# Performance work log

Hardware: AMD Instinct MI355X
Metric: run time of the kernel (lower is better)

The kernel has to match this reference:

```python
import jax, jax.numpy as jnp
import numpy as np

H = 1024; NH = 16; L = 4; K = 128; N = 65536
ADIM_MOVE = 9; ADIM_TURN = 4; S = 2 * K + 2


def setup_inputs() -> dict:
    key = jax.random.key(0)
    ks = jax.random.split(key, 24)
    s = 0.02
    d = {}
    d['x'] = jax.random.normal(ks[0], (1, H), jnp.float32)
    d['memory_vectors'] = jax.random.normal(ks[1], (N, H), jnp.float32)
    d['memory_next_vectors'] = jax.random.normal(ks[2], (N, H), jnp.float32)
    d['memory_surprises'] = jax.random.uniform(ks[3], (N,), jnp.float32)
    d['memory_rewards'] = jax.random.normal(ks[4], (N,), jnp.float32)
    d['rand_noise'] = jax.random.uniform(ks[5], (N,), jnp.float32)
    d['action_idx_move'] = jax.random.randint(ks[6], (N,), 0, ADIM_MOVE)
    d['action_idx_turn'] = jax.random.randint(ks[7], (N,), 0, ADIM_TURN)
    d['start_token'] = jax.random.uniform(ks[8], (1, H)) * 2 - 1
    d['pos_emb'] = jax.random.uniform(ks[9], (S, H)) * 2 - 1
    d['in_proj_w'] = jax.random.normal(ks[10], (L, 3 * H, H)) * s
    d['in_proj_b'] = jnp.zeros((L, 3 * H))
    d['out_w'] = jax.random.normal(ks[11], (L, H, H)) * s
    d['out_b'] = jnp.zeros((L, H))
    d['ln1_w'] = jnp.ones((L, H)); d['ln1_b'] = jnp.zeros((L, H))
    d['ln2_w'] = jnp.ones((L, H)); d['ln2_b'] = jnp.zeros((L, H))
    d['ffn_w1'] = jax.random.normal(ks[12], (L, 4 * H, H)) * s
    d['ffn_b1'] = jnp.zeros((L, 4 * H))
    d['ffn_w2'] = jax.random.normal(ks[13], (L, H, 4 * H)) * s
    d['ffn_b2'] = jnp.zeros((L, H))
    d['act_move_w1'] = jax.random.normal(ks[14], (H, ADIM_MOVE)) * s
    d['act_move_b1'] = jnp.zeros((H,))
    d['act_move_w2'] = jax.random.normal(ks[15], (H, H)) * s
    d['act_move_b2'] = jnp.zeros((H,))
    d['act_turn_w1'] = jax.random.normal(ks[16], (H, ADIM_TURN)) * s
    d['act_turn_b1'] = jnp.zeros((H,))
    d['act_turn_w2'] = jax.random.normal(ks[17], (H, H)) * s
    d['act_turn_b2'] = jnp.zeros((H,))
    d['vh_w1'] = jax.random.normal(ks[18], (4 * H, H)) * s
    d['vh_b1'] = jnp.zeros((4 * H,))
    d['vh_w2'] = jax.random.normal(ks[19], (1, 4 * H)) * s
    d['vh_b2'] = jnp.zeros((1,))
    return d


def _get_scores(v):
    # tie-aware average rank / N (matches torch unique_consecutive logic)
    srt = jnp.sort(v)
    left = jnp.searchsorted(srt, v, side='left')
    right = jnp.searchsorted(srt, v, side='right')
    return ((left + right - 1).astype(v.dtype) / 2) / v.shape[0]


def _ln(x, w, b):
    m = x.mean(-1, keepdims=True)
    var = ((x - m) ** 2).mean(-1, keepdims=True)
    return (x - m) / jnp.sqrt(var + 1e-5) * w + b


def _gelu(x):
    return jax.nn.gelu(x, approximate=False)


def _mha(x, wqkv, bqkv, wo, bo, mask):
    dh = H // NH
    qkv = x @ wqkv.T + bqkv                      # [S, 3H]
    q, k, v = jnp.split(qkv, 3, axis=-1)
    q = q.reshape(-1, NH, dh); k = k.reshape(-1, NH, dh); v = v.reshape(-1, NH, dh)
    att = jnp.einsum('qhd,khd->hqk', q, k) / np.sqrt(dh).astype(np.float32)
    att = jax.nn.softmax(att + mask, axis=-1)
    o = jnp.einsum('hqk,khd->qhd', att, v).reshape(-1, H)
    return o @ wo.T + bo


def reference(x, memory_vectors, memory_next_vectors, memory_surprises, memory_rewards, rand_noise, action_idx_move, action_idx_turn, start_token, pos_emb, in_proj_w, in_proj_b, out_w, out_b, ln1_w, ln1_b, ln2_w, ln2_b, ffn_w1, ffn_b1, ffn_w2, ffn_b2, act_move_w1, act_move_b1, act_move_w2, act_move_b2, act_turn_w1, act_turn_b1, act_turn_w2, act_turn_b2, vh_w1, vh_b1, vh_w2, vh_b2):
    eps = 1e-8
    # ---- scoring (no_grad in original) ----
    xs = jax.lax.stop_gradient(x)
    xn = xs / jnp.maximum(jnp.linalg.norm(xs, axis=-1, keepdims=True), eps)
    mn = memory_vectors / jnp.maximum(jnp.linalg.norm(memory_vectors, axis=-1, keepdims=True), eps)
    sim = mn @ xn[0]                              # [N]
    scores = _get_scores(memory_surprises) ** 2 + _get_scores(sim) ** 2 + _get_scores(rand_noise) ** 2
    _, idx = jax.lax.top_k(scores, K)             # [K]
    # ---- gather memories + action one-hots ----
    sel = jax.lax.stop_gradient(memory_vectors[idx])   # [K, H]
    oh_move = jax.nn.one_hot(action_idx_move[idx], ADIM_MOVE, dtype=x.dtype)
    oh_turn = jax.nn.one_hot(action_idx_turn[idx], ADIM_TURN, dtype=x.dtype)
    av_move = _gelu(oh_move @ act_move_w1.T + act_move_b1) @ act_move_w2.T + act_move_b2
    av_turn = _gelu(oh_turn @ act_turn_w1.T + act_turn_b1) @ act_turn_w2.T + act_turn_b2
    av = (av_move + av_turn) / 2                  # mean over actions
    # interleave [v0, a0, v1, a1, ...], prepend start, append target
    vecs = jnp.stack((sel, av), axis=1).reshape(-1, H)
    vecs = jnp.concatenate((start_token, vecs, x), axis=0)   # [S, H]
    vecs = vecs + pos_emb
    mask = jnp.where(jnp.tril(jnp.ones((S, S), bool)), 0.0, -jnp.inf).astype(x.dtype)
    for l in range(L):
        vecs = vecs + _mha(_ln(vecs, ln1_w[l], ln1_b[l]), in_proj_w[l], in_proj_b[l], out_w[l], out_b[l], mask)
        h = _ln(vecs, ln2_w[l], ln2_b[l])
        vecs = vecs + _gelu(h @ ffn_w1[l].T + ffn_b1[l]) @ ffn_w2[l].T + ffn_b2[l]
    vidx = jnp.arange(K + 1) * 2 + 1
    vh_in = vecs[vidx]
    vp = _gelu(vh_in @ vh_w1.T + vh_b1) @ vh_w2.T + vh_b2   # [K+1, 1]
    sel_rewards = memory_rewards[idx]
    losses = (vp[:-1].ravel() - sel_rewards) ** 2            # mse, reduction='none'
    return (vecs[1:], memory_next_vectors[idx], vp[-1], losses, sel_rewards)
```

## Files before the change

### kernel.cpp

```cpp
#include <hip/hip_runtime.h>
#include <hip/hip_bf16.h>
#include <math.h>
#include <stdint.h>

typedef unsigned int u32;
typedef unsigned short u16;
typedef unsigned long long u64;

#define NM   65536
#define HD   1024
#define KS   128
#define SQ   258
#define NL   4
#define NBIN 65536
#define CCAP 2048

using bf16x8 = __attribute__((ext_vector_type(8))) short;
using f32x4v = __attribute__((ext_vector_type(4))) float;

static constexpr size_t A256(size_t x){ return (x + 255) & ~(size_t)255; }

constexpr size_t OFF_H3   = 0;
constexpr size_t OFF_C3   = OFF_H3 + (size_t)3*NBIN*4;
constexpr size_t OFF_HS   = OFF_C3 + (size_t)3*NBIN*4;
constexpr size_t ZERO_BYTES = OFF_HS + (size_t)NBIN*4;
constexpr u32 ZBLK = 1792;
constexpr size_t OFF_BS   = A256(ZERO_BYTES);
constexpr size_t OFF_P3   = A256(OFF_BS + 192*4);
constexpr size_t OFF_K3   = A256(OFF_P3 + (size_t)3*(NBIN+1)*4);
constexpr size_t OFF_L3   = A256(OFF_K3 + (size_t)3*NM*4);
constexpr size_t OFF_KSC  = A256(OFF_L3 + (size_t)3*NM*2);
constexpr size_t OFF_IDX  = A256(OFF_KSC + (size_t)NM*4);
constexpr size_t OFF_REW  = A256(OFF_IDX  + (size_t)KS*4);
constexpr size_t OFF_HM   = A256(OFF_REW  + (size_t)KS*4);
constexpr size_t OFF_HT   = A256(OFF_HM   + (size_t)KS*HD*2);
constexpr size_t OFF_VECS = A256(OFF_HT   + (size_t)KS*HD*2);
// ... 209 lines not shown
      if(cum + c >= (u32)KS){ thrT = (u32)(base+j) << 16; cnt = 0; break; }
      cum += c;
    }
  }
  __syncthreads();
  u32 T = thrT;
  for(int i=t;i<NM;i+=1024){
    u32 k = keysS[i];
    if(k >= T){
      u32 p = atomicAdd(&cnt, 1u);
      if(p < (u32)CCAP) sm[p] = ((u64)(~k) << 32) | (u32)i;
    }
  }
  __syncthreads();
  u32 n = cnt; if(n > (u32)CCAP) n = CCAP;
  for(int i=t;i<CCAP;i+=1024) if(i >= (int)n) sm[i] = 0xFFFFFFFFFFFFFFFFull;
  __syncthreads();
  for(int k=2;k<=CCAP;k<<=1){
    for(int j=k>>1;j>0;j>>=1){
      for(int i=t;i<CCAP;i+=1024){
        int ixj = i ^ j;
        if(ixj > i){
          bool up = ((i & k) == 0);
          u64 a = sm[i], b = sm[ixj];
          if((a > b) == up){ sm[i] = b; sm[ixj] = a; }
        }
      }
      __syncthreads();
    }
  }
  if(t < KS) idx[t] = (int)(sm[t] & 0xFFFFFFFFu);
}

__global__ void k_gather(const int* __restrict__ idx,
                         const float* __restrict__ mv, const float* __restrict__ mnv,
                         const float* __restrict__ mrew,
                         const int* __restrict__ aim, const int* __restrict__ ait,
                         const float* __restrict__ amw1, const float* __restrict__ amb1,
                         const float* __restrict__ atw1, const float* __restrict__ atb1,
                         const float* __restrict__ start, const float* __restrict__ x,
                         const float* __restrict__ pos,
                         float* __restrict__ vecs, float* __restrict__ outnext,
                         u16* __restrict__ hm, u16* __restrict__ ht,
                         float* __restrict__ rew, float* __restrict__ outrew){
  int k = blockIdx.x;
  int t = threadIdx.x;
  if(k < KS){
    int row = idx[k];
    const float4* a = (const float4*)(mv  + (size_t)row*HD);
    const float4* b = (const float4*)(mnv + (size_t)row*HD);
    const float4* pz = (const float4*)(pos + (size_t)(2*k+1)*HD);
    float4* vr = (float4*)(vecs + (size_t)(2*k+1)*HD);
    float4* on = (float4*)(outnext + (size_t)k*HD);
    float4 av = a[t], bv = b[t], pv = pz[t];
    av.x += pv.x; av.y += pv.y; av.z += pv.z; av.w += pv.w;
    vr[t] = av; on[t] = bv;
    int am = aim[row], at = ait[row];
    for(int j=t;j<HD;j+=256){
      hm[(size_t)k*HD+j] = f2bf(gelu_f(amw1[(size_t)j*9 + am] + amb1[j]));
      ht[(size_t)k*HD+j] = f2bf(gelu_f(atw1[(size_t)j*4 + at] + atb1[j]));
    }
    if(t == 0){ float r = mrew[row]; rew[k] = r; outrew[k] = r; }
  } else {
    const float4* st = (const float4*)start;
    const float4* xx = (const float4*)x;
    const float4* p0 = (const float4*)pos;
    const float4* p1 = (const float4*)(pos + (size_t)(SQ-1)*HD);
    float4 v0 = st[t], v1 = xx[t], q0 = p0[t], q1 = p1[t];
    v0.x += q0.x; v0.y += q0.y; v0.z += q0.z; v0.w += q0.w;
    v1.x += q1.x; v1.y += q1.y; v1.z += q1.z; v1.w += q1.w;
    ((float4*)vecs)[t] = v0;
    ((float4*)(vecs + (size_t)(SQ-1)*HD))[t] = v1;
  }
}

__device__ __forceinline__ void gemm_body(u16* As, u16* Bs, const u16* __restrict__ A, const u16* __restrict__ B,
        u16* __restrict__ P, int M, int N, int K, int S, int nbm, int lda, int tile){
  int bm = (tile % nbm) * 64;
  int tmp = tile / nbm;
  int z  = tmp % S;
  int bn = (tmp / S) * 64;
  int Ks = K / S, kbeg = z*Ks;
  int nk = Ks >> 6;

  int t = threadIdx.x, lane = t & 63, w = t >> 6;
  int s0 = w*64 + lane, s1 = s0 + 256;
  int r0s = s0 >> 3, c0s = (s0 & 7) ^ (r0s & 7);
  int r1s = s1 >> 3, c1s = (s1 & 7) ^ (r1s & 7);
  const u16* ga0 = A + (size_t)(bm + r0s)*lda + kbeg + c0s*8;
  const u16* ga1 = A + (size_t)(bm + r1s)*lda + kbeg + c1s*8;
  const u16* gb0 = B + (size_t)(bn + r0s)*K  + kbeg + c0s*8;
  const u16* gb1 = B + (size_t)(bn + r1s)*K  + kbeg + c1s*8;
  int lb0 = w*512, lb1 = 2048 + w*512;

  int wm = (w >> 1)*32, wn = (w & 1)*32;
  int lr = lane & 15, lg = lane >> 4;
  int ra0 = wm + lr, ra1 = ra0 + 16;
  int rb0 = wn + lr, rb1 = rb0 + 16;
  int a00 = ra0*64 + ((lg     ^ (ra0&7))*8);
  int a01 = ra0*64 + (((4+lg) ^ (ra0&7))*8);
  int a10 = ra1*64 + ((lg     ^ (ra1&7))*8);
  int a11 = ra1*64 + (((4+lg) ^ (ra1&7))*8);
  int b00 = rb0*64 + ((lg     ^ (rb0&7))*8);
  int b01 = rb0*64 + (((4+lg) ^ (rb0&7))*8);
  int b10 = rb1*64 + ((lg     ^ (rb1&7))*8);
  int b11 = rb1*64 + (((4+lg) ^ (rb1&7))*8);

  f32x4v acc00 = {0,0,0,0}, acc01 = {0,0,0,0}, acc10 = {0,0,0,0}, acc11 = {0,0,0,0};

// ... 16 lines not shown
    bf16x8 xb1 = *(const bf16x8*)&Bs[cur + b10];
    acc00 = __builtin_amdgcn_mfma_f32_16x16x32_bf16(xa0, xb0, acc00, 0, 0, 0);
    acc01 = __builtin_amdgcn_mfma_f32_16x16x32_bf16(xa0, xb1, acc01, 0, 0, 0);
    acc10 = __builtin_amdgcn_mfma_f32_16x16x32_bf16(xa1, xb0, acc10, 0, 0, 0);
    acc11 = __builtin_amdgcn_mfma_f32_16x16x32_bf16(xa1, xb1, acc11, 0, 0, 0);
    xa0 = *(const bf16x8*)&As[cur + a01];
    xa1 = *(const bf16x8*)&As[cur + a11];
    xb0 = *(const bf16x8*)&Bs[cur + b01];
    xb1 = *(const bf16x8*)&Bs[cur + b11];
    acc00 = __builtin_amdgcn_mfma_f32_16x16x32_bf16(xa0, xb0, acc00, 0, 0, 0);
    acc01 = __builtin_amdgcn_mfma_f32_16x16x32_bf16(xa0, xb1, acc01, 0, 0, 0);
    acc10 = __builtin_amdgcn_mfma_f32_16x16x32_bf16(xa1, xb0, acc10, 0, 0, 0);
    acc11 = __builtin_amdgcn_mfma_f32_16x16x32_bf16(xa1, xb1, acc11, 0, 0, 0);
    __syncthreads();
  }

  size_t zbase = (size_t)z * (size_t)M;
  #pragma unroll
  for(int r=0;r<4;++r){
    int row0 = bm + wm + lg*4 + r;
    int row1 = row0 + 16;
    int cc0 = bn + wn + lr, cc1 = cc0 + 16;
    if(row0 < M){
      P[(zbase+row0)*N + cc0] = f2bf(acc00[r]);
      P[(zbase+row0)*N + cc1] = f2bf(acc01[r]);
    }
    if(row1 < M){
      P[(zbase+row1)*N + cc0] = f2bf(acc10[r]);
      P[(zbase+row1)*N + cc1] = f2bf(acc11[r]);
    }
  }
}

__global__ __launch_bounds__(256) void k_gemm(const u16* __restrict__ A, const u16* __restrict__ B,
        u16* __restrict__ P, int M, int N, int K, int S, int nbm, int lda){
  __shared__ u16 As[8192];
  __shared__ u16 Bs[8192];
  u32 nwg = gridDim.x, orig = blockIdx.x;
  u32 swz = (orig & 7)*(nwg >> 3) + (orig >> 3);
  gemm_body(As, Bs, A, B, P, M, N, K, S, nbm, lda, (int)swz);
}

__global__ __launch_bounds__(256) void k_actgemm(const u16* __restrict__ hm, const u16* __restrict__ ht,
        const u16* __restrict__ amw2, const u16* __restrict__ atw2,
        u16* __restrict__ part, u16* __restrict__ part2){
  __shared__ u16 As[8192];
  __shared__ u16 Bs[8192];
  int which = blockIdx.x >> 8, tile = blockIdx.x & 255;
  gemm_body(As, Bs, which ? ht : hm, which ? atw2 : amw2, which ? part2 : part,
            KS, HD, HD, 8, 2, HD, tile);
}

template<int S_, int ACT, bool BFOUT>
__global__ __launch_bounds__(256) void k_finS(const u16* __restrict__ P, const float* __restrict__ bias,
                                              float* __restrict__ C, u16* __restrict__ Cb, int MN4, int Nd){
  int i4 = blockIdx.x*256 + threadIdx.x;
  if(i4 >= MN4) return;
  size_t off = (size_t)i4*4;
  size_t MN = (size_t)MN4*4;
  float4 v = unpk4(*(const u64*)&P[off]);
  #pragma unroll
  for(int z=1;z<S_;++z){
    float4 q = unpk4(*(const u64*)&P[(size_t)z*MN + off]);
    v.x += q.x; v.y += q.y; v.z += q.z; v.w += q.w;
  }
  int j = (i4 % (Nd/4))*4;
  float4 b4 = *(const float4*)&bias[j];
  v.x += b4.x; v.y += b4.y; v.z += b4.z; v.w += b4.w;
  if(ACT == 1){ v.x = gelu_f(v.x); v.y = gelu_f(v.y); v.z = gelu_f(v.z); v.w = gelu_f(v.w); }
  if(BFOUT) *(u64*)&Cb[off] = pk4(v);
  else      *(float4*)&C[off] = v;
}

template<int S_, bool LN>
__global__ __launch_bounds__(256) void k_finrow(const u16* __restrict__ P, const float* __restrict__ bias,
                                                float* __restrict__ vecs, const float* __restrict__ lw,
                                                const float* __restrict__ lb, u16* __restrict__ lnb,
                                                float* __restrict__ outp, u16* __restrict__ vhin){
  __shared__ float red[256];
  int row = blockIdx.x, t = threadIdx.x;
  int j = t*4;
  float4 v = unpk4(*(const u64*)&P[(size_t)row*HD + j]);
  #pragma unroll
  for(int z=1;z<S_;++z){
    float4 p = unpk4(*(const u64*)&P[((size_t)z*SQ + row)*HD + j]);
    v.x += p.x; v.y += p.y; v.z += p.z; v.w += p.w;
  }
  float4 b4 = *(const float4*)&bias[j];
  float4 r4 = *(const float4*)&vecs[(size_t)row*HD + j];
  v.x += b4.x + r4.x; v.y += b4.y + r4.y; v.z += b4.z + r4.z; v.w += b4.w + r4.w;
  *(float4*)&vecs[(size_t)row*HD + j] = v;
  if(LN){
    red[t] = v.x+v.y+v.z+v.w; __syncthreads();
    for(int o=128;o>0;o>>=1){ if(t<o) red[t]+=red[t+o]; __syncthreads(); }
    float m = red[0]*(1.0f/HD); __syncthreads();
    float dx=v.x-m, dy=v.y-m, dz=v.z-m, dw=v.w-m;
    red[t] = dx*dx+dy*dy+dz*dz+dw*dw; __syncthreads();
    for(int o=128;o>0;o>>=1){ if(t<o) red[t]+=red[t+o]; __syncthreads(); }
    float den = sqrtf(red[0]*(1.0f/HD) + 1e-5f);
    float4 w4 = *(const float4*)&lw[j];
    float4 lb4 = *(const float4*)&lb[j];
    float4 o4;
    o4.x = dx/den*w4.x + lb4.x; o4.y = dy/den*w4.y + lb4.y;
    o4.z = dz/den*w4.z + lb4.z; o4.w = dw/den*w4.w + lb4.w;
    *(u64*)&lnb[(size_t)row*HD + j] = pk4(o4);
  } else {
    if(row >= 1) *(float4*)&outp[(size_t)(row-1)*HD + j] = v;
    if(row & 1){
      int vr = (row-1) >> 1;
      *(u64*)&vhin[(size_t)vr*HD + j] = pk4(v);
    }
  }
}

__global__ __launch_bounds__(256) void k_finavln(const u16* __restrict__ Pm, const u16* __restrict__ Pt,
                                                 const float* __restrict__ bm_, const float* __restrict__ bt_,
                                                 const float* __restrict__ pos, float* __restrict__ vecs,
                                                 const float* __restrict__ lw, const float* __restrict__ lb,
                                                 u16* __restrict__ lnb){
  __shared__ float red[256];
  int row = blockIdx.x, t = threadIdx.x;
  int j = t*4;
  float4 v;
  if(row >= 2 && row <= 256 && ((row & 1) == 0)){
    int k = (row-2) >> 1;
    float4 s = {0,0,0,0};
    #pragma unroll
    for(int z=0;z<8;++z){
      float4 a = unpk4(*(const u64*)&Pm[((size_t)z*KS + k)*HD + j]);
      float4 b = unpk4(*(const u64*)&Pt[((size_t)z*KS + k)*HD + j]);
      s.x += a.x+b.x; s.y += a.y+b.y; s.z += a.z+b.z; s.w += a.w+b.w;
    }
    float4 bm4 = *(const float4*)&bm_[j];
    float4 bt4 = *(const float4*)&bt_[j];
    float4 p4 = *(const float4*)&pos[(size_t)row*HD + j];
    v.x = 0.5f*(s.x + bm4.x + bt4.x) + p4.x;
    v.y = 0.5f*(s.y + bm4.y + bt4.y) + p4.y;
    v.z = 0.5f*(s.z + bm4.z + bt4.z) + p4.z;
    v.w = 0.5f*(s.w + bm4.w + bt4.w) + p4.w;
    *(float4*)&vecs[(size_t)row*HD + j] = v;
  } else {
    v = *(const float4*)&vecs[(size_t)row*HD + j];
  }
  red[t] = v.x+v.y+v.z+v.w; __syncthreads();
  for(int o=128;o>0;o>>=1){ if(t<o) red[t]+=red[t+o]; __syncthreads(); }
  float m = red[0]*(1.0f/HD); __syncthreads();
  float dx=v.x-m, dy=v.y-m, dz=v.z-m, dw=v.w-m;
  red[t] = dx*dx+dy*dy+dz*dz+dw*dw; __syncthreads();
  for(int o=128;o>0;o>>=1){ if(t<o) red[t]+=red[t+o]; __syncthreads(); }
  float den = sqrtf(red[0]*(1.0f/HD) + 1e-5f);
  float4 w4 = *(const float4*)&lw[j];
  float4 lb4 = *(const float4*)&lb[j];
  float4 o4;
  o4.x = dx/den*w4.x + lb4.x; o4.y = dy/den*w4.y + lb4.y;
  o4.z = dz/den*w4.z + lb4.z; o4.w = dw/den*w4.w + lb4.w;
  *(u64*)&lnb[(size_t)row*HD + j] = pk4(o4);
}

__global__ void k_attn(const u16* __restrict__ qkv, u16* __restrict__ outp){
  __shared__ float qv[64];
  __shared__ float p[SQ];
  __shared__ float red[256];
  int q = blockIdx.x, h = blockIdx.y, t = threadIdx.x;
  if(t < 64) qv[t] = bf2f(qkv[(size_t)q*3072 + h*64 + t]);
  __syncthreads();
  int nk = q + 1;
  float lmax = -1e30f;
  for(int j=t;j<nk;j+=256){
    const u32* kr = (const u32*)(qkv + (size_t)j*3072 + 1024 + h*64);
    float d = 0.f;
    #pragma unroll
    for(int c2=0;c2<32;++c2){
      u32 pk = kr[c2];
      d += qv[c2*2]   * __uint_as_float(pk << 16);
      d += qv[c2*2+1] * __uint_as_float(pk & 0xFFFF0000u);
    }
    d *= 0.125f;
    p[j] = d;
    lmax = fmaxf(lmax, d);
  }
  red[t] = lmax; __syncthreads();
  for(int o=128;o>0;o>>=1){ if(t<o) red[t] = fmaxf(red[t], red[t+o]); __syncthreads(); }
  float m = red[0];
  __syncthreads();
  float lsum = 0.f;
  for(int j=t;j<nk;j+=256){ float e = expf(p[j]-m); p[j] = e; lsum += e; }
  red[t] = lsum; __syncthreads();
  for(int o=128;o>0;o>>=1){ if(t<o) red[t] += red[t+o]; __syncthreads(); }
  float inv = 1.0f/red[0];
  __syncthreads();
  int d = t & 63, g = t >> 6;
  float acc = 0.f;
  for(int j=g;j<nk;j+=4) acc += p[j]*bf2f(qkv[(size_t)j*3072 + 2048 + h*64 + d]);
  red[t] = acc; __syncthreads();
  if(g == 0){
    float o4 = red[d] + red[64+d] + red[128+d] + red[192+d];
    outp[(size_t)q*HD + h*64 + d] = f2bf(o4*inv);
  }
}

__global__ __launch_bounds__(256) void k_vpfin(const u16* __restrict__ P, const float* __restrict__ vb1,
                                               const float* __restrict__ vw2, const float* __restrict__ vb2,
                                               const float* __restrict__ rew, float* __restrict__ outp){
  __shared__ float red[256];
  int r = blockIdx.x, t = threadIdx.x;
  float s = 0.f;
  for(int c4=t;c4<1024;c4+=256){
    float4 v = unpk4(*(const u64*)&P[(size_t)r*4096 + c4*4]);
    #pragma unroll
    for(int z=1;z<4;++z){
      float4 q = unpk4(*(const u64*)&P[((size_t)z*129 + r)*4096 + c4*4]);
      v.x += q.x; v.y += q.y; v.z += q.z; v.w += q.w;
    }
    float4 b4 = *(const float4*)&vb1[c4*4];
    float4 w4 = *(const float4*)&vw2[c4*4];
    s += gelu_f(v.x + b4.x)*w4.x + gelu_f(v.y + b4.y)*w4.y
       + gelu_f(v.z + b4.z)*w4.z + gelu_f(v.w + b4.w)*w4.w;
  }
  red[t]=s; __syncthreads();
  for(int o=128;o>0;o>>=1){ if(t<o) red[t]+=red[t+o]; __syncthreads(); }
  if(t == 0){
    float val = red[0] + vb2[0];
    if(r == KS) outp[OUT_VP] = val;
    else { float d = val - rew[r]; outp[OUT_LOSS + r] = d*d; }
  }
}

extern "C" void kernel_launch(void* const* d_in, const int* in_sizes, int n_in,
                              void* d_out, int out_size, void* d_ws, size_t ws_size,
                              hipStream_t stream){
  const float* x     = (const float*)d_in[0];
  const float* mv    = (const float*)d_in[1];
  const float* mnv   = (const float*)d_in[2];
  const float* surp  = (const float*)d_in[3];
  const float* mrew  = (const float*)d_in[4];
  const float* noise = (const float*)d_in[5];
  const int*   aim   = (const int*)d_in[6];
  const int*   ait   = (const int*)d_in[7];
  const float* start = (const float*)d_in[8];
  const float* pos   = (const float*)d_in[9];
  const float* inW = (const float*)d_in[10]; const float* inB = (const float*)d_in[11];
  const float* oW  = (const float*)d_in[12]; const float* oB  = (const float*)d_in[13];
  const float* l1w = (const float*)d_in[14]; const float* l1b = (const float*)d_in[15];
  const float* l2w = (const float*)d_in[16]; const float* l2b = (const float*)d_in[17];
  const float* f1w = (const float*)d_in[18]; const float* f1b = (const float*)d_in[19];
  const float* f2w = (const float*)d_in[20]; const float* f2b = (const float*)d_in[21];
  const float* amw1= (const float*)d_in[22]; const float* amb1= (const float*)d_in[23];
  const float* amw2= (const float*)d_in[24]; const float* amb2= (const float*)d_in[25];
  const float* atw1= (const float*)d_in[26]; const float* atb1= (const float*)d_in[27];
  const float* atw2= (const float*)d_in[28]; const float* atb2= (const float*)d_in[29];
  const float* vw1 = (const float*)d_in[30]; const float* vb1 = (const float*)d_in[31];
  const float* vw2 = (const float*)d_in[32]; const float* vb2 = (const float*)d_in[33];

  float* out = (float*)d_out;
  char* ws = (char*)d_ws;
  u32*  hist3 = (u32*)(ws+OFF_H3);
  u32*  cnt3  = (u32*)(ws+OFF_C3);
  u32*  histS = (u32*)(ws+OFF_HS);
  u32*  bsum  = (u32*)(ws+OFF_BS);
  u32*  pref3 = (u32*)(ws+OFF_P3);
  u32*  keys3 = (u32*)(ws+OFF_K3);
  u16*  lo3   = (u16*)(ws+OFF_L3);
  u32*  keysS = (u32*)(ws+OFF_KSC);
  int*  idxb  = (int*)(ws+OFF_IDX);
  float* rew  = (float*)(ws+OFF_REW);
  u16*  hm    = (u16*)(ws+OFF_HM);
  u16*  ht    = (u16*)(ws+OFF_HT);
  float* vecs = (float*)(ws+OFF_VECS);
  u16*  lnb   = (u16*)(ws+OFF_LNB);
  u16*  qkvb  = (u16*)(ws+OFF_QKV);
  u16*  attn  = (u16*)(ws+OFF_ATT);
  u16*  ffh   = (u16*)(ws+OFF_FFH);
  u16*  vhin  = (u16*)(ws+OFF_VHIN);
  u16*  wb    = (u16*)(ws+OFF_WB);
  u16*  part  = (u16*)(ws+OFF_PART);
  u16*  part2 = part + (size_t)8*KS*HD;

  u16* inW_bf = wb + WB_IN;
  u16* oW_bf  = wb + WB_O;
  u16* f1w_bf = wb + WB_F1;
  u16* f2w_bf = wb + WB_F2;
  u16* am_bf  = wb + WB_AM;
  u16* at_bf  = wb + WB_AT;
  u16* vh_bf  = wb + WB_VH;

  dim3 b256(256);
  int gN = NM/256;

  {
    WCA a;
    const float* srcs[7] = { inW, oW, f1w, f2w, amw2, atw2, vw1 };
    u16* dsts[7] = { inW_bf, oW_bf, f1w_bf, f2w_bf, am_bf, at_bf, vh_bf };
    u32 sizes4[7] = { 4*3*HD*HD/4, 4*HD*HD/4, 4*4*HD*HD/4, 4*4*HD*HD/4, HD*HD/4, HD*HD/4, 4*HD*HD/4 };
    u32 cum = 0;
    for(int j=0;j<7;++j){
      a.seg[j].s = srcs[j]; a.seg[j].d = dsts[j];
      a.seg[j].base4 = cum; cum += sizes4[j]; a.seg[j].end4 = cum;
    }
    a.tot4 = cum;
    a.z = (u32*)ws;
    hipLaunchKernelGGL(k_wconv, dim3((cum + 255)/256), b256, 0, stream, a);
  }

  hipLaunchKernelGGL(k_simkey, dim3(NM/8), b256, 0, stream, mv, x, surp, noise, keys3, hist3);
  hipLaunchKernelGGL(k_scanA, dim3(192), b256, 0, stream, hist3, bsum);
  hipLaunchKernelGGL(k_scanC, dim3(192), b256, 0, stream, hist3, bsum, pref3);
  hipLaunchKernelGGL(k_scatter3, dim3(gN), b256, 0, stream, keys3, pref3, cnt3, lo3);
  hipLaunchKernelGGL(k_rank3score, dim3(gN), b256, 0, stream, keys3, pref3, lo3, keysS, histS);
  hipLaunchKernelGGL(k_selsort, dim3(1), dim3(1024), 0, stream, histS, keysS, idxb);

  hipLaunchKernelGGL(k_gather, dim3(KS+1), b256, 0, stream, idxb, mv, mnv, mrew, aim, ait,
                     amw1, amb1, atw1, atb1, start, x, pos,
                     vecs, out + OUT_NEXT, hm, ht, rew, out + OUT_REWO);
  hipLaunchKernelGGL(k_actgemm, dim3(512), b256, 0, stream, hm, ht, am_bf, at_bf, part, part2);
  hipLaunchKernelGGL(k_finavln, dim3(SQ), b256, 0, stream, part, part2, amb2, atb2, pos, vecs, l1w, l1b, lnb);

  for(int l=0;l<NL;++l){
    hipLaunchKernelGGL(k_gemm, dim3(480), b256, 0, stream, lnb, inW_bf + (size_t)l*3*HD*HD, part, SQ, 3*HD, HD, 2, 5, HD);
    hipLaunchKernelGGL((k_finS<2,0,true>), dim3(774), b256, 0, stream, part, inB + (size_t)l*3*HD, (float*)nullptr, qkvb, SQ*3*HD/4, 3*HD);
    hipLaunchKernelGGL(k_attn, dim3(SQ, 16), b256, 0, stream, qkvb, attn);
    hipLaunchKernelGGL(k_gemm, dim3(640), b256, 0, stream, attn, oW_bf + (size_t)l*HD*HD, part, SQ, HD, HD, 8, 5, HD);
    hipLaunchKernelGGL((k_finrow<8,true>), dim3(SQ), b256, 0, stream, part, oB + (size_t)l*HD, vecs,
                       l2w + (size_t)l*HD, l2b + (size_t)l*HD, lnb, (float*)nullptr, (u16*)nullptr);
    hipLaunchKernelGGL(k_gemm, dim3(640), b256, 0, stream, lnb, f1w_bf + (size_t)l*4*HD*HD, part, SQ, 4*HD, HD, 2, 5, HD);
    hipLaunchKernelGGL((k_finS<2,1,true>), dim3(1032), b256, 0, stream, part, f1b + (size_t)l*4*HD, (float*)nullptr, ffh, SQ*4*HD/4, 4*HD);
    hipLaunchKernelGGL(k_gemm, dim3(640), b256, 0, stream, ffh, f2w_bf + (size_t)l*HD*4*HD, part, SQ, HD, 4*HD, 8, 5, 4*HD);
    if(l < NL-1)
      hipLaunchKernelGGL((k_finrow<8,true>), dim3(SQ), b256, 0, stream, part, f2b + (size_t)l*HD, vecs,
                         l1w + (size_t)(l+1)*HD, l1b + (size_t)(l+1)*HD, lnb, (float*)nullptr, (u16*)nullptr);
    else
      hipLaunchKernelGGL((k_finrow<8,false>), dim3(SQ), b256, 0, stream, part, f2b + (size_t)l*HD, vecs,
                         (const float*)nullptr, (const float*)nullptr, (u16*)nullptr, out, vhin);
  }

  hipLaunchKernelGGL(k_gemm, dim3(768), b256, 0, stream, vhin, vh_bf, part, KS+1, 4*HD, HD, 4, 3, HD);
  hipLaunchKernelGGL(k_vpfin, dim3(KS+1), b256, 0, stream, part, vb1, vw2, vb2, rew, out);
}
```

Measured before the change: 850.5 us.

## Fuse transformer stages into one persistent cooperative kernel with grid syncs

```diff
diff --git a/kernel.cpp b/kernel.cpp
--- a/kernel.cpp
+++ b/kernel.cpp
@@ -1,7 +1,10 @@
 #include <hip/hip_runtime.h>
+#include <hip/hip_cooperative_groups.h>
 #include <hip/hip_bf16.h>
 #include <math.h>
 #include <stdint.h>
+
+namespace cg = cooperative_groups;
 
 typedef unsigned int u32;
 typedef unsigned short u16;
@@ -277,49 +280,48 @@
   if(t < KS) idx[t] = (int)(sm[t] & 0xFFFFFFFFu);
 }
 
-__global__ void k_gather(const int* __restrict__ idx,
-                         const float* __restrict__ mv, const float* __restrict__ mnv,
-                         const float* __restrict__ mrew,
-                         const int* __restrict__ aim, const int* __restrict__ ait,
-                         const float* __restrict__ amw1, const float* __restrict__ amb1,
-                         const float* __restrict__ atw1, const float* __restrict__ atb1,
-                         const float* __restrict__ start, const float* __restrict__ x,
-                         const float* __restrict__ pos,
-                         float* __restrict__ vecs, float* __restrict__ outnext,
-                         u16* __restrict__ hm, u16* __restrict__ ht,
-                         float* __restrict__ rew, float* __restrict__ outrew){
-  int k = blockIdx.x;
-  int t = threadIdx.x;
+struct CP {
+  const int* idx;
+  const float *mv,*mnv,*mrew;
+  const int *aim,*ait;
+  const float *amw1,*amb1,*atw1,*atb1,*start,*x,*pos;
+  float *vecs,*out,*rew;
+  u16 *hm,*ht,*lnb,*qkvb,*attn,*ffh,*vhin,*part,*part2;
+  const u16 *amw2b,*atw2b,*inWb,*oWb,*f1wb,*f2wb,*vhwb;
+  const float *amb2,*atb2,*inB,*oB,*f1b,*f2b,*l1w,*l1b,*l2w,*l2b,*vb1,*vw2,*vb2;
+};
+
+__device__ void gather_dev(const CP& p, int k, int t){
   if(k < KS){
-    int row = idx[k];
-    const float4* a = (const float4*)(mv  + (size_t)row*HD);
-    const float4* b = (const float4*)(mnv + (size_t)row*HD);
-    const float4* pz = (const float4*)(pos + (size_t)(2*k+1)*HD);
-    float4* vr = (float4*)(vecs + (size_t)(2*k+1)*HD);
-    float4* on = (float4*)(outnext + (size_t)k*HD);
+    int row = p.idx[k];
+    const float4* a = (const float4*)(p.mv  + (size_t)row*HD);
+    const float4* b = (const float4*)(p.mnv + (size_t)row*HD);
+    const float4* pz = (const float4*)(p.pos + (size_t)(2*k+1)*HD);
+    float4* vr = (float4*)(p.vecs + (size_t)(2*k+1)*HD);
+    float4* on = (float4*)(p.out + OUT_NEXT + (size_t)k*HD);
     float4 av = a[t], bv = b[t], pv = pz[t];
     av.x += pv.x; av.y += pv.y; av.z += pv.z; av.w += pv.w;
     vr[t] = av; on[t] = bv;
-    int am = aim[row], at = ait[row];
+    int am = p.aim[row], at = p.ait[row];
     for(int j=t;j<HD;j+=256){
-      hm[(size_t)k*HD+j] = f2bf(gelu_f(amw1[(size_t)j*9 + am] + amb1[j]));
-      ht[(size_t)k*HD+j] = f2bf(gelu_f(atw1[(size_t)j*4 + at] + atb1[j]));
-    }
-    if(t == 0){ float r = mrew[row]; rew[k] = r; outrew[k] = r; }
+      p.hm[(size_t)k*HD+j] = f2bf(gelu_f(p.amw1[(size_t)j*9 + am] + p.amb1[j]));
+      p.ht[(size_t)k*HD+j] = f2bf(gelu_f(p.atw1[(size_t)j*4 + at] + p.atb1[j]));
+    }
+    if(t == 0){ float r = p.mrew[row]; p.rew[k] = r; p.out[OUT_REWO + k] = r; }
   } else {
-    const float4* st = (const float4*)start;
-    const float4* xx = (const float4*)x;
-    const float4* p0 = (const float4*)pos;
-    const float4* p1 = (const float4*)(pos + (size_t)(SQ-1)*HD);
+    const float4* st = (const float4*)p.start;
+    const float4* xx = (const float4*)p.x;
+    const float4* p0 = (const float4*)p.pos;
+    const float4* p1 = (const float4*)(p.pos + (size_t)(SQ-1)*HD);
     float4 v0 = st[t], v1 = xx[t], q0 = p0[t], q1 = p1[t];
     v0.x += q0.x; v0.y += q0.y; v0.z += q0.z; v0.w += q0.w;
     v1.x += q1.x; v1.y += q1.y; v1.z += q1.z; v1.w += q1.w;
-    ((float4*)vecs)[t] = v0;
-    ((float4*)(vecs + (size_t)(SQ-1)*HD))[t] = v1;
-  }
-}
-
-__device__ __forceinline__ void gemm_body(u16* As, u16* Bs, const u16* __restrict__ A, const u16* __restrict__ B,
+    ((float4*)p.vecs)[t] = v0;
+    ((float4*)(p.vecs + (size_t)(SQ-1)*HD))[t] = v1;
+  }
+}
+
+__device__ void gemm_tile(u16* As, u16* Bs, const u16* __restrict__ A, const u16* __restrict__ B,
         u16* __restrict__ P, int M, int N, int K, int S, int nbm, int lda, int tile){
   int bm = (tile % nbm) * 64;
   int tmp = tile / nbm;
@@ -402,32 +404,10 @@
   }
 }
 
-__global__ __launch_bounds__(256) void k_gemm(const u16* __restrict__ A, const u16* __restrict__ B,
-        u16* __restrict__ P, int M, int N, int K, int S, int nbm, int lda){
-  __shared__ u16 As[8192];
-  __shared__ u16 Bs[8192];
-  u32 nwg = gridDim.x, orig = blockIdx.x;
-  u32 swz = (orig & 7)*(nwg >> 3) + (orig >> 3);
-  gemm_body(As, Bs, A, B, P, M, N, K, S, nbm, lda, (int)swz);
-}
-
-__global__ __launch_bounds__(256) void k_actgemm(const u16* __restrict__ hm, const u16* __restrict__ ht,
-        const u16* __restrict__ amw2, const u16* __restrict__ atw2,
-        u16* __restrict__ part, u16* __restrict__ part2){
-  __shared__ u16 As[8192];
-  __shared__ u16 Bs[8192];
-  int which = blockIdx.x >> 8, tile = blockIdx.x & 255;
-  gemm_body(As, Bs, which ? ht : hm, which ? atw2 : amw2, which ? part2 : part,
-            KS, HD, HD, 8, 2, HD, tile);
-}
-
-template<int S_, int ACT, bool BFOUT>
-__global__ __launch_bounds__(256) void k_finS(const u16* __restrict__ P, const float* __restrict__ bias,
-                                              float* __restrict__ C, u16* __restrict__ Cb, int MN4, int Nd){
-  int i4 = blockIdx.x*256 + threadIdx.x;
-  if(i4 >= MN4) return;
+template<int S_, int ACT>
+__device__ __forceinline__ void finS_dev(const u16* __restrict__ P, const float* __restrict__ bias,
+                                         u16* __restrict__ Cb, int i4, size_t MN, int Nd){
   size_t off = (size_t)i4*4;
-  size_t MN = (size_t)MN4*4;
   float4 v = unpk4(*(const u64*)&P[off]);
   #pragma unroll
   for(int z=1;z<S_;++z){
@@ -438,17 +418,15 @@
   float4 b4 = *(const float4*)&bias[j];
   v.x += b4.x; v.y += b4.y; v.z += b4.z; v.w += b4.w;
   if(ACT == 1){ v.x = gelu_f(v.x); v.y = gelu_f(v.y); v.z = gelu_f(v.z); v.w = gelu_f(v.w); }
-  if(BFOUT) *(u64*)&Cb[off] = pk4(v);
-  else      *(float4*)&C[off] = v;
+  *(u64*)&Cb[off] = pk4(v);
 }
 
 template<int S_, bool LN>
-__global__ __launch_bounds__(256) void k_finrow(const u16* __restrict__ P, const float* __restrict__ bias,
-                                                float* __restrict__ vecs, const float* __restrict__ lw,
-                                                const float* __restrict__ lb, u16* __restrict__ lnb,
-                                                float* __restrict__ outp, u16* __restrict__ vhin){
-  __shared__ float red[256];
-  int row = blockIdx.x, t = threadIdx.x;
+__device__ void finrow_dev(const u16* __restrict__ P, const float* __restrict__ bias,
+                           float* __restrict__ vecs, const float* __restrict__ lw,
+                           const float* __restrict__ lb, u16* __restrict__ lnb,
+                           float* __restrict__ outp, u16* __restrict__ vhin,
+                           float* red, int row, int t){
   int j = t*4;
   float4 v = unpk4(*(const u64*)&P[(size_t)row*HD + j]);
   #pragma unroll
@@ -468,6 +446,7 @@
     red[t] = dx*dx+dy*dy+dz*dz+dw*dw; __syncthreads();
     for(int o=128;o>0;o>>=1){ if(t<o) red[t]+=red[t+o]; __syncthreads(); }
     float den = sqrtf(red[0]*(1.0f/HD) + 1e-5f);
+    __syncthreads();
     float4 w4 = *(const float4*)&lw[j];
     float4 lb4 = *(const float4*)&lb[j];
     float4 o4;
@@ -483,13 +462,7 @@
   }
 }
 
-__global__ __launch_bounds__(256) void k_finavln(const u16* __restrict__ Pm, const u16* __restrict__ Pt,
-                                                 const float* __restrict__ bm_, const float* __restrict__ bt_,
-                                                 const float* __restrict__ pos, float* __restrict__ vecs,
-                                                 const float* __restrict__ lw, const float* __restrict__ lb,
-                                                 u16* __restrict__ lnb){
-  __shared__ float red[256];
-  int row = blockIdx.x, t = threadIdx.x;
+__device__ void finavln_dev(const CP& p, float* red, int row, int t){
   int j = t*4;
   float4 v;
   if(row >= 2 && row <= 256 && ((row & 1) == 0)){
@@ -497,20 +470,20 @@
     float4 s = {0,0,0,0};
     #pragma unroll
     for(int z=0;z<8;++z){
-      float4 a = unpk4(*(const u64*)&Pm[((size_t)z*KS + k)*HD + j]);
-      float4 b = unpk4(*(const u64*)&Pt[((size_t)z*KS + k)*HD + j]);
+      float4 a = unpk4(*(const u64*)&p.part [((size_t)z*KS + k)*HD + j]);
+      float4 b = unpk4(*(const u64*)&p.part2[((size_t)z*KS + k)*HD + j]);
       s.x += a.x+b.x; s.y += a.y+b.y; s.z += a.z+b.z; s.w += a.w+b.w;
     }
-    float4 bm4 = *(const float4*)&bm_[j];
-    float4 bt4 = *(const float4*)&bt_[j];
-    float4 p4 = *(const float4*)&pos[(size_t)row*HD + j];
+    float4 bm4 = *(const float4*)&p.amb2[j];
+    float4 bt4 = *(const float4*)&p.atb2[j];
+    float4 p4 = *(const float4*)&p.pos[(size_t)row*HD + j];
     v.x = 0.5f*(s.x + bm4.x + bt4.x) + p4.x;
     v.y = 0.5f*(s.y + bm4.y + bt4.y) + p4.y;
     v.z = 0.5f*(s.z + bm4.z + bt4.z) + p4.z;
     v.w = 0.5f*(s.w + bm4.w + bt4.w) + p4.w;
-    *(float4*)&vecs[(size_t)row*HD + j] = v;
+    *(float4*)&p.vecs[(size_t)row*HD + j] = v;
   } else {
-    v = *(const float4*)&vecs[(size_t)row*HD + j];
+    v = *(const float4*)&p.vecs[(size_t)row*HD + j];
   }
   red[t] = v.x+v.y+v.z+v.w; __syncthreads();
   for(int o=128;o>0;o>>=1){ if(t<o) red[t]+=red[t+o]; __syncthreads(); }
@@ -519,81 +492,191 @@
   red[t] = dx*dx+dy*dy+dz*dz+dw*dw; __syncthreads();
   for(int o=128;o>0;o>>=1){ if(t<o) red[t]+=red[t+o]; __syncthreads(); }
   float den = sqrtf(red[0]*(1.0f/HD) + 1e-5f);
-  float4 w4 = *(const float4*)&lw[j];
-  float4 lb4 = *(const float4*)&lb[j];
+  __syncthreads();
+  float4 w4 = *(const float4*)&p.l1w[j];
+  float4 lb4 = *(const float4*)&p.l1b[j];
   float4 o4;
   o4.x = dx/den*w4.x + lb4.x; o4.y = dy/den*w4.y + lb4.y;
   o4.z = dz/den*w4.z + lb4.z; o4.w = dw/den*w4.w + lb4.w;
-  *(u64*)&lnb[(size_t)row*HD + j] = pk4(o4);
-}
-
-__global__ void k_attn(const u16* __restrict__ qkv, u16* __restrict__ outp){
-  __shared__ float qv[64];
-  __shared__ float p[SQ];
-  __shared__ float red[256];
-  int q = blockIdx.x, h = blockIdx.y, t = threadIdx.x;
-  if(t < 64) qv[t] = bf2f(qkv[(size_t)q*3072 + h*64 + t]);
-  __syncthreads();
+  *(u64*)&p.lnb[(size_t)row*HD + j] = pk4(o4);
+}
+
+__device__ void attn_dev(const u16* __restrict__ qkv, u16* __restrict__ outp, int task, int t, char* smem){
+  int team = t >> 6, lane = t & 63;
+  int q = task >> 2, h = (task & 3)*4 + team;
+  float* qs = (float*)smem + team*64;
+  float* pl = (float*)(smem + 1024) + team*264;
   int nk = q + 1;
-  float lmax = -1e30f;
-  for(int j=t;j<nk;j+=256){
-    const u32* kr = (const u32*)(qkv + (size_t)j*3072 + 1024 + h*64);
-    float d = 0.f;
-    #pragma unroll
-    for(int c2=0;c2<32;++c2){
-      u32 pk = kr[c2];
-      d += qv[c2*2]   * __uint_as_float(pk << 16);
-      d += qv[c2*2+1] * __uint_as_float(pk & 0xFFFF0000u);
-    }
-    d *= 0.125f;
-    p[j] = d;
-    lmax = fmaxf(lmax, d);
-  }
-  red[t] = lmax; __syncthreads();
-  for(int o=128;o>0;o>>=1){ if(t<o) red[t] = fmaxf(red[t], red[t+o]); __syncthreads(); }
-  float m = red[0];
-  __syncthreads();
-  float lsum = 0.f;
-  for(int j=t;j<nk;j+=256){ float e = expf(p[j]-m); p[j] = e; lsum += e; }
-  red[t] = lsum; __syncthreads();
-  for(int o=128;o>0;o>>=1){ if(t<o) red[t] += red[t+o]; __syncthreads(); }
-  float inv = 1.0f/red[0];
-  __syncthreads();
-  int d = t & 63, g = t >> 6;
+  qs[lane] = bf2f(qkv[(size_t)q*3072 + h*64 + lane]);
+  float pv[5]; float mx = -1e30f;
+  #pragma unroll
+  for(int rep=0;rep<5;++rep){
+    int j = lane + rep*64;
+    float s = -1e30f;
+    if(j < nk){
+      const u32* kr = (const u32*)(qkv + (size_t)j*3072 + 1024 + h*64);
+      float d = 0.f;
+      #pragma unroll
+      for(int c2=0;c2<32;++c2){
+        u32 pk = kr[c2];
+        d += qs[c2*2]   * __uint_as_float(pk << 16);
+        d += qs[c2*2+1] * __uint_as_float(pk & 0xFFFF0000u);
+      }
+      s = d*0.125f;
+    }
+    pv[rep] = s; mx = fmaxf(mx, s);
+  }
+  for(int o=32;o>0;o>>=1) mx = fmaxf(mx, __shfl_xor(mx,o,64));
+  float sum = 0.f;
+  #pragma unroll
+  for(int rep=0;rep<5;++rep){
+    int j = lane + rep*64;
+    if(j < nk){ float e = expf(pv[rep]-mx); pl[j] = e; sum += e; }
+  }
+  for(int o=32;o>0;o>>=1) sum += __shfl_xor(sum,o,64);
+  float inv = 1.0f/sum;
   float acc = 0.f;
-  for(int j=g;j<nk;j+=4) acc += p[j]*bf2f(qkv[(size_t)j*3072 + 2048 + h*64 + d]);
-  red[t] = acc; __syncthreads();
-  if(g == 0){
-    float o4 = red[d] + red[64+d] + red[128+d] + red[192+d];
-    outp[(size_t)q*HD + h*64 + d] = f2bf(o4*inv);
-  }
-}
-
-__global__ __launch_bounds__(256) void k_vpfin(const u16* __restrict__ P, const float* __restrict__ vb1,
-                                               const float* __restrict__ vw2, const float* __restrict__ vb2,
-                                               const float* __restrict__ rew, float* __restrict__ outp){
-  __shared__ float red[256];
-  int r = blockIdx.x, t = threadIdx.x;
+  for(int j=0;j<nk;++j) acc += pl[j]*bf2f(qkv[(size_t)j*3072 + 2048 + h*64 + lane]);
+  outp[(size_t)q*HD + h*64 + lane] = f2bf(acc*inv);
+}
+
+__device__ void vpfin_dev(const CP& p, float* red, int r, int t){
   float s = 0.f;
   for(int c4=t;c4<1024;c4+=256){
-    float4 v = unpk4(*(const u64*)&P[(size_t)r*4096 + c4*4]);
+    float4 v = unpk4(*(const u64*)&p.part[(size_t)r*4096 + c4*4]);
     #pragma unroll
     for(int z=1;z<4;++z){
-      float4 q = unpk4(*(const u64*)&P[((size_t)z*129 + r)*4096 + c4*4]);
+      float4 q = unpk4(*(const u64*)&p.part[((size_t)z*129 + r)*4096 + c4*4]);
       v.x += q.x; v.y += q.y; v.z += q.z; v.w += q.w;
     }
-    float4 b4 = *(const float4*)&vb1[c4*4];
-    float4 w4 = *(const float4*)&vw2[c4*4];
+    float4 b4 = *(const float4*)&p.vb1[c4*4];
+    float4 w4 = *(const float4*)&p.vw2[c4*4];
     s += gelu_f(v.x + b4.x)*w4.x + gelu_f(v.y + b4.y)*w4.y
        + gelu_f(v.z + b4.z)*w4.z + gelu_f(v.w + b4.w)*w4.w;
   }
   red[t]=s; __syncthreads();
   for(int o=128;o>0;o>>=1){ if(t<o) red[t]+=red[t+o]; __syncthreads(); }
   if(t == 0){
-    float val = red[0] + vb2[0];
-    if(r == KS) outp[OUT_VP] = val;
-    else { float d = val - rew[r]; outp[OUT_LOSS + r] = d*d; }
-  }
+    float val = red[0] + p.vb2[0];
+    if(r == KS) p.out[OUT_VP] = val;
+    else { float d = val - p.rew[r]; p.out[OUT_LOSS + r] = d*d; }
+  }
+  __syncthreads();
+}
+
+__global__ __launch_bounds__(256, 4) void k_coop(CP p){
+  cg::grid_group grid = cg::this_grid();
+  __shared__ char smem[33792];
+  u16* As = (u16*)smem;
+  u16* Bs = (u16*)(smem + 16384);
+  float* red = (float*)(smem + 32768);
+  const int bid = blockIdx.x, t = threadIdx.x;
+  const int NB = gridDim.x;
+
+  for(int k=bid; k<KS+1; k+=NB) gather_dev(p, k, t);
+  grid.sync();
+  for(int task=bid; task<512; task+=NB){
+    int which = task >> 8, tl = task & 255;
+    gemm_tile(As, Bs, which ? p.ht : p.hm, which ? p.atw2b : p.amw2b,
+              which ? p.part2 : p.part, KS, HD, HD, 8, 2, HD, tl);
+  }
+  grid.sync();
+  for(int row=bid; row<SQ; row+=NB) finavln_dev(p, red, row, t);
+  grid.sync();
+
+  for(int l=0;l<NL;++l){
+    const u16* inW = p.inWb + (size_t)l*3*HD*HD;
+    for(int task=bid; task<960; task+=NB)
+      gemm_tile(As, Bs, p.lnb, inW, p.part, SQ, 3*HD, HD, 4, 5, HD, task);
+    grid.sync();
+    for(int i4=bid*256+t; i4 < SQ*3*HD/4; i4 += NB*256)
+      finS_dev<4,0>(p.part, p.inB + (size_t)l*3*HD, p.qkvb, i4, (size_t)SQ*3*HD, 3*HD);
+    grid.sync();
+    for(int task=bid; task<SQ*4; task+=NB) attn_dev(p.qkvb, p.attn, task, t, smem);
+    grid.sync();
+    const u16* oW = p.oWb + (size_t)l*HD*HD;
+    for(int task=bid; task<640; task+=NB)
+      gemm_tile(As, Bs, p.attn, oW, p.part, SQ, HD, HD, 8, 5, HD, task);
+    grid.sync();
+    for(int row=bid; row<SQ; row+=NB)
+      finrow_dev<8,true>(p.part, p.oB + (size_t)l*HD, p.vecs,
+                         p.l2w + (size_t)l*HD, p.l2b + (size_t)l*HD, p.lnb,
+                         nullptr, nullptr, red, row, t);
+    grid.sync();
+    const u16* f1w = p.f1wb + (size_t)l*4*HD*HD;
+    for(int task=bid; task<640; task+=NB)
+      gemm_tile(As, Bs, p.lnb, f1w, p.part, SQ, 4*HD, HD, 2, 5, HD, task);
+    grid.sync();
+    for(int i4=bid*256+t; i4 < SQ*4*HD/4; i4 += NB*256)
+      finS_dev<2,1>(p.part, p.f1b + (size_t)l*4*HD, p.ffh, i4, (size_t)SQ*4*HD, 4*HD);
+    grid.sync();
+    const u16* f2w = p.f2wb + (size_t)l*HD*4*HD;
+    for(int task=bid; task<640; task+=NB)
+      gemm_tile(As, Bs, p.ffh, f2w, p.part, SQ, HD, 4*HD, 8, 5, 4*HD, task);
+    grid.sync();
+    if(l < NL-1){
+      for(int row=bid; row<SQ; row+=NB)
+        finrow_dev<8,true>(p.part, p.f2b + (size_t)l*HD, p.vecs,
+                           p.l1w + (size_t)(l+1)*HD, p.l1b + (size_t)(l+1)*HD, p.lnb,
+                           nullptr, nullptr, red, row, t);
+    } else {
+      for(int row=bid; row<SQ; row+=NB)
+        finrow_dev<8,false>(p.part, p.f2b + (size_t)l*HD, p.vecs,
+                            nullptr, nullptr, nullptr, p.out, p.vhin, red, row, t);
+    }
+    grid.sync();
+  }
+
+  for(int task=bid; task<768; task+=NB)
+    gemm_tile(As, Bs, p.vhin, p.vhwb, p.part, KS+1, 4*HD, HD, 4, 3, HD, task);
+  grid.sync();
+  for(int r=bid; r<KS+1; r+=NB) vpfin_dev(p, red, r, t);
+}
+
+__global__ void k_gatherW(CP p){ gather_dev(p, blockIdx.x, threadIdx.x); }
+
+__global__ __launch_bounds__(256) void k_actgemmW(CP p){
+  __shared__ u16 As[8192]; __shared__ u16 Bs[8192];
+  int which = blockIdx.x >> 8, tl = blockIdx.x & 255;
+  gemm_tile(As, Bs, which ? p.ht : p.hm, which ? p.atw2b : p.amw2b,
+            which ? p.part2 : p.part, KS, HD, HD, 8, 2, HD, tl);
+}
+
+__global__ __launch_bounds__(256) void k_finavlnW(CP p){
+  __shared__ float red[256];
+  finavln_dev(p, red, blockIdx.x, threadIdx.x);
+}
+
+__global__ __launch_bounds__(256) void k_gemmW(const u16* __restrict__ A, const u16* __restrict__ B,
+        u16* __restrict__ P, int M, int N, int K, int S, int nbm, int lda){
+  __shared__ u16 As[8192]; __shared__ u16 Bs[8192];
+  u32 nwg = gridDim.x, orig = blockIdx.x;
+  u32 swz = (orig & 7)*(nwg >> 3) + (orig >> 3);
+  gemm_tile(As, Bs, A, B, P, M, N, K, S, nbm, lda, (int)swz);
+}
+
+template<int S_, int ACT>
+__global__ __launch_bounds__(256) void k_finSW(const u16* P, const float* bias, u16* Cb, int MN4, int Nd){
+  int i4 = blockIdx.x*256 + threadIdx.x;
+  if(i4 >= MN4) return;
+  finS_dev<S_,ACT>(P, bias, Cb, i4, (size_t)MN4*4, Nd);
+}
+
+__global__ void k_attnW(const u16* qkv, u16* outp){
+  __shared__ char smem[5248];
+  attn_dev(qkv, outp, blockIdx.x, threadIdx.x, smem);
+}
+
+template<int S_, bool LN>
+__global__ __launch_bounds__(256) void k_finrowW(const u16* P, const float* bias, float* vecs,
+        const float* lw, const float* lb, u16* lnb, float* outp, u16* vhin){
+  __shared__ float red[256];
+  finrow_dev<S_,LN>(P, bias, vecs, lw, lb, lnb, outp, vhin, red, blockIdx.x, threadIdx.x);
+}
+
+__global__ __launch_bounds__(256) void k_vpfinW(CP p){
+  __shared__ float red[256];
+  vpfin_dev(p, red, blockIdx.x, threadIdx.x);
 }
 
 extern "C" void kernel_launch(void* const* d_in, const int* in_sizes, int n_in,
@@ -633,26 +716,28 @@
   u16*  lo3   = (u16*)(ws+OFF_L3);
   u32*  keysS = (u32*)(ws+OFF_KSC);
   int*  idxb  = (int*)(ws+OFF_IDX);
-  float* rew  = (float*)(ws+OFF_REW);
-  u16*  hm    = (u16*)(ws+OFF_HM);
-  u16*  ht    = (u16*)(ws+OFF_HT);
-  float* vecs = (float*)(ws+OFF_VECS);
-  u16*  lnb   = (u16*)(ws+OFF_LNB);
-  u16*  qkvb  = (u16*)(ws+OFF_QKV);
-  u16*  attn  = (u16*)(ws+OFF_ATT);
-  u16*  ffh   = (u16*)(ws+OFF_FFH);
-  u16*  vhin  = (u16*)(ws+OFF_VHIN);
-  u16*  wb    = (u16*)(ws+OFF_WB);
-  u16*  part  = (u16*)(ws+OFF_PART);
-  u16*  part2 = part + (size_t)8*KS*HD;
-
-  u16* inW_bf = wb + WB_IN;
-  u16* oW_bf  = wb + WB_O;
-  u16* f1w_bf = wb + WB_F1;
-  u16* f2w_bf = wb + WB_F2;
-  u16* am_bf  = wb + WB_AM;
-  u16* at_bf  = wb + WB_AT;
-  u16* vh_bf  = wb + WB_VH;
+
+  CP cp;
+  cp.idx = idxb;
+  cp.mv = mv; cp.mnv = mnv; cp.mrew = mrew;
+  cp.aim = aim; cp.ait = ait;
+  cp.amw1 = amw1; cp.amb1 = amb1; cp.atw1 = atw1; cp.atb1 = atb1;
+  cp.start = start; cp.x = x; cp.pos = pos;
+  cp.vecs = (float*)(ws+OFF_VECS);
+  cp.out = out;
+  cp.rew = (float*)(ws+OFF_REW);
+  cp.hm = (u16*)(ws+OFF_HM); cp.ht = (u16*)(ws+OFF_HT);
+  cp.lnb = (u16*)(ws+OFF_LNB); cp.qkvb = (u16*)(ws+OFF_QKV);
+  cp.attn = (u16*)(ws+OFF_ATT); cp.ffh = (u16*)(ws+OFF_FFH);
+  cp.vhin = (u16*)(ws+OFF_VHIN);
+  cp.part = (u16*)(ws+OFF_PART);
+  cp.part2 = cp.part + (size_t)8*KS*HD;
+  u16* wb = (u16*)(ws+OFF_WB);
+  cp.inWb = wb + WB_IN; cp.oWb = wb + WB_O; cp.f1wb = wb + WB_F1; cp.f2wb = wb + WB_F2;
+  cp.amw2b = wb + WB_AM; cp.atw2b = wb + WB_AT; cp.vhwb = wb + WB_VH;
+  cp.amb2 = amb2; cp.atb2 = atb2; cp.inB = inB; cp.oB = oB;
+  cp.f1b = f1b; cp.f2b = f2b; cp.l1w = l1w; cp.l1b = l1b; cp.l2w = l2w; cp.l2b = l2b;
+  cp.vb1 = vb1; cp.vw2 = vw2; cp.vb2 = vb2;
 
   dim3 b256(256);
   int gN = NM/256;
@@ -660,7 +745,8 @@
   {
     WCA a;
     const float* srcs[7] = { inW, oW, f1w, f2w, amw2, atw2, vw1 };
-    u16* dsts[7] = { inW_bf, oW_bf, f1w_bf, f2w_bf, am_bf, at_bf, vh_bf };
+    u16* dsts[7] = { (u16*)cp.inWb, (u16*)cp.oWb, (u16*)cp.f1wb, (u16*)cp.f2wb,
+                     (u16*)cp.amw2b, (u16*)cp.atw2b, (u16*)cp.vhwb };
     u32 sizes4[7] = { 4*3*HD*HD/4, 4*HD*HD/4, 4*4*HD*HD/4, 4*4*HD*HD/4, HD*HD/4, HD*HD/4, 4*HD*HD/4 };
     u32 cum = 0;
     for(int j=0;j<7;++j){
@@ -679,30 +765,34 @@
   hipLaunchKernelGGL(k_rank3score, dim3(gN), b256, 0, stream, keys3, pref3, lo3, keysS, histS);
   hipLaunchKernelGGL(k_selsort, dim3(1), dim3(1024), 0, stream, histS, keysS, idxb);
 
-  hipLaunchKernelGGL(k_gather, dim3(KS+1), b256, 0, stream, idxb, mv, mnv, mrew, aim, ait,
-                     amw1, amb1, atw1, atb1, start, x, pos,
-                     vecs, out + OUT_NEXT, hm, ht, rew, out + OUT_REWO);
-  hipLaunchKernelGGL(k_actgemm, dim3(512), b256, 0, stream, hm, ht, am_bf, at_bf, part, part2);
-  hipLaunchKernelGGL(k_finavln, dim3(SQ), b256, 0, stream, part, part2, amb2, atb2, pos, vecs, l1w, l1b, lnb);
-
-  for(int l=0;l<NL;++l){
-    hipLaunchKernelGGL(k_gemm, dim3(480), b256, 0, stream, lnb, inW_bf + (size_t)l*3*HD*HD, part, SQ, 3*HD, HD, 2, 5, HD);
-    hipLaunchKernelGGL((k_finS<2,0,true>), dim3(774), b256, 0, stream, part, inB + (size_t)l*3*HD, (float*)nullptr, qkvb, SQ*3*HD/4, 3*HD);
-    hipLaunchKernelGGL(k_attn, dim3(SQ, 16), b256, 0, stream, qkvb, attn);
-    hipLaunchKernelGGL(k_gemm, dim3(640), b256, 0, stream, attn, oW_bf + (size_t)l*HD*HD, part, SQ, HD, HD, 8, 5, HD);
-    hipLaunchKernelGGL((k_finrow<8,true>), dim3(SQ), b256, 0, stream, part, oB + (size_t)l*HD, vecs,
-                       l2w + (size_t)l*HD, l2b + (size_t)l*HD, lnb, (float*)nullptr, (u16*)nullptr);
-    hipLaunchKernelGGL(k_gemm, dim3(640), b256, 0, stream, lnb, f1w_bf + (size_t)l*4*HD*HD, part, SQ, 4*HD, HD, 2, 5, HD);
-    hipLaunchKernelGGL((k_finS<2,1,true>), dim3(1032), b256, 0, stream, part, f1b + (size_t)l*4*HD, (float*)nullptr, ffh, SQ*4*HD/4, 4*HD);
-    hipLaunchKernelGGL(k_gemm, dim3(640), b256, 0, stream, ffh, f2w_bf + (size_t)l*HD*4*HD, part, SQ, HD, 4*HD, 8, 5, 4*HD);
-    if(l < NL-1)
-      hipLaunchKernelGGL((k_finrow<8,true>), dim3(SQ), b256, 0, stream, part, f2b + (size_t)l*HD, vecs,
-                         l1w + (size_t)(l+1)*HD, l1b + (size_t)(l+1)*HD, lnb, (float*)nullptr, (u16*)nullptr);
-    else
-      hipLaunchKernelGGL((k_finrow<8,false>), dim3(SQ), b256, 0, stream, part, f2b + (size_t)l*HD, vecs,
-                         (const float*)nullptr, (const float*)nullptr, (u16*)nullptr, out, vhin);
-  }
-
-  hipLaunchKernelGGL(k_gemm, dim3(768), b256, 0, stream, vhin, vh_bf, part, KS+1, 4*HD, HD, 4, 3, HD);
-  hipLaunchKernelGGL(k_vpfin, dim3(KS+1), b256, 0, stream, part, vb1, vw2, vb2, rew, out);
-}
+  int occ = 0;
+  (void)hipOccupancyMaxActiveBlocksPerMultiprocessor(&occ, k_coop, 256, 0);
+  int nb = occ * 256; if(nb > 1024) nb = 1024;
+  if(nb >= 256){
+    void* args[] = { &cp };
+    (void)hipLaunchCooperativeKernel((const void*)k_coop, dim3(nb), dim3(256), args, 0, stream);
+  } else {
+    hipLaunchKernelGGL(k_gatherW, dim3(KS+1), b256, 0, stream, cp);
+    hipLaunchKernelGGL(k_actgemmW, dim3(512), b256, 0, stream, cp);
+    hipLaunchKernelGGL(k_finavlnW, dim3(SQ), b256, 0, stream, cp);
+    for(int l=0;l<NL;++l){
+      hipLaunchKernelGGL(k_gemmW, dim3(960), b256, 0, stream, cp.lnb, cp.inWb + (size_t)l*3*HD*HD, cp.part, SQ, 3*HD, HD, 4, 5, HD);
+      hipLaunchKernelGGL((k_finSW<4,0>), dim3(774), b256, 0, stream, cp.part, inB + (size_t)l*3*HD, cp.qkvb, SQ*3*HD/4, 3*HD);
+      hipLaunchKernelGGL(k_attnW, dim3(SQ*4), b256, 0, stream, cp.qkvb, cp.attn);
+      hipLaunchKernelGGL(k_gemmW, dim3(640), b256, 0, stream, cp.attn, cp.oWb + (size_t)l*HD*HD, cp.part, SQ, HD, HD, 8, 5, HD);
+      hipLaunchKernelGGL((k_finrowW<8,true>), dim3(SQ), b256, 0, stream, cp.part, oB + (size_t)l*HD, cp.vecs,
+                         l2w + (size_t)l*HD, l2b + (size_t)l*HD, cp.lnb, (float*)nullptr, (u16*)nullptr);
+      hipLaunchKernelGGL(k_gemmW, dim3(640), b256, 0, stream, cp.lnb, cp.f1wb + (size_t)l*4*HD*HD, cp.part, SQ, 4*HD, HD, 2, 5, HD);
+      hipLaunchKernelGGL((k_finSW<2,1>), dim3(1032), b256, 0, stream, cp.part, f1b + (size_t)l*4*HD, cp.ffh, SQ*4*HD/4, 4*HD);
+      hipLaunchKernelGGL(k_gemmW, dim3(640), b256, 0, stream, cp.ffh, cp.f2wb + (size_t)l*HD*4*HD, cp.part, SQ, HD, 4*HD, 8, 5, 4*HD);
+      if(l < NL-1)
+        hipLaunchKernelGGL((k_finrowW<8,true>), dim3(SQ), b256, 0, stream, cp.part, f2b + (size_t)l*HD, cp.vecs,
+                           l1w + (size_t)(l+1)*HD, l1b + (size_t)(l+1)*HD, cp.lnb, (float*)nullptr, (u16*)nullptr);
+      else
+        hipLaunchKernelGGL((k_finrowW<8,false>), dim3(SQ), b256, 0, stream, cp.part, f2b + (size_t)l*HD, cp.vecs,
+                           (const float*)nullptr, (const float*)nullptr, (u16*)nullptr, out, cp.vhin);
+    }
+    hipLaunchKernelGGL(k_gemmW, dim3(768), b256, 0, stream, cp.vhin, cp.vhwb, cp.part, KS+1, 4*HD, HD, 4, 3, HD);
+    hipLaunchKernelGGL(k_vpfinW, dim3(KS+1), b256, 0, stream, cp);
+  }
+}
```

New measurement: 3.218 ms. 278% more time.
